# Optimization experiments

Measured on AMD Instinct MI355X. Metric: run time of the kernel, lower is better.

## Reference

```python
import jax, jax.numpy as jnp
import numpy as np

B, L, R = 4, 2048, 1024        # batch, seq_len, residual_dim
HID, EXP, K = 64, 2, 3          # hidden_dim, expansion_factor, conv_kernel_size
D = HID * EXP                   # ssm_input_dim = 128
N = HID                         # SSM state size = 64


def setup_inputs() -> dict:
    key = jax.random.key(0)
    ks = jax.random.split(key, 16)
    g = lambda k, s: jax.random.normal(k, s, dtype=jnp.float32) * 0.02
    inp = {
        "up_x":   jax.random.normal(ks[0], (B, L, R), dtype=jnp.float32),
        "W_up":   g(ks[1], (R, 2 * D)),
        "b_up":   g(ks[2], (2 * D,)),
        "conv_w": g(ks[3], (D, K)),          # depthwise Conv1d weight [C,1,K] squeezed
        "conv_b": g(ks[4], (D,)),
        "W_delta": g(ks[5], (D, D)),
        "b_delta": g(ks[6], (D,)),
        "W_B":    g(ks[7], (D, N)),
        "b_B":    g(ks[8], (N,)),
        "W_C":    g(ks[9], (D, N)),
        "b_C":    g(ks[10], (N,)),
        "A_log":  jnp.log(jnp.broadcast_to(jnp.arange(1, N + 1, dtype=jnp.float32), (D, N))),
        "D_skip": jnp.ones((D,), dtype=jnp.float32),
        "W_down": g(ks[11], (D, R)),
        "b_down": g(ks[12], (R,)),
    }
    return inp


def reference(up_x, W_up, b_up, conv_w, conv_b, W_delta, b_delta,
              W_B, b_B, W_C, b_C, A_log, D_skip, W_down, b_down):
    Lq = up_x.shape[1]
    u = up_x @ W_up + b_up                               # [B,L,2D]
    left, right = jnp.split(u, 2, axis=-1)               # each [B,L,D]

    # causal depthwise conv (pad left K-1, truncate to L)
    xp = jnp.pad(left, ((0, 0), (K - 1, 0), (0, 0)))     # [B,L+K-1,D]
    conv = sum(conv_w[:, k] * xp[:, k:k + Lq, :] for k in range(K)) + conv_b
    x = jax.nn.silu(conv)                                # [B,L,D]

    # S6 selective scan
    delta = jax.nn.softplus(x @ W_delta + b_delta)       # [B,L,D]
    Bm = x @ W_B + b_B                                   # [B,L,N]
    Cm = x @ W_C + b_C                                   # [B,L,N]
    A = -jnp.exp(A_log)                                  # [D,N]
    dA = jnp.exp(delta[..., None] * A)                   # [B,L,D,N]
    dBx = delta[..., None] * Bm[:, :, None, :] * x[..., None]  # [B,L,D,N]

    def step(h, inputs):
        dA_t, dBx_t, C_t = inputs                        # [B,D,N],[B,D,N],[B,N]
        h = dA_t * h + dBx_t
        y_t = jnp.einsum('bdn,bn->bd', h, C_t)
        return h, y_t

    h0 = jnp.zeros((up_x.shape[0], D, N), dtype=x.dtype)
    _, ys = jax.lax.scan(step, h0, (jnp.swapaxes(dA, 0, 1),
                                    jnp.swapaxes(dBx, 0, 1),
                                    jnp.swapaxes(Cm, 0, 1)))
    y = jnp.swapaxes(ys, 0, 1) + D_skip * x              # [B,L,D]

    gated = y * jax.nn.silu(right)                       # SiLU gate
    return gated @ W_down + b_down                       # [B,L,R]
```

## Files before the change

### kernel.cpp

```cpp
#include <hip/hip_runtime.h>
#include <math.h>

#define B_ 4
#define L_ 2048
#define R_ 1024
#define D_ 128
#define N_ 64
#define TWO_D 256
#define M_ (B_*L_)

#define LSTR 68

typedef __attribute__((ext_vector_type(8))) short bf16x8;
typedef __attribute__((ext_vector_type(4))) float f32x4;

__device__ __forceinline__ float silu_f(float z) {
    return z / (1.0f + __expf(-z));
}

__device__ __forceinline__ float softplus_f(float z) {
    return fmaxf(z, 0.0f) + log1pf(__expf(-fabsf(z)));
}

__device__ __forceinline__ short f2bf(float f) {
    union { float f; unsigned int u; } v; v.f = f;
    unsigned int r = v.u + 0x7FFF + ((v.u >> 16) & 1);
    return (short)(r >> 16);
}

__device__ __forceinline__ bf16x8 pack8(float4 a, float4 b) {
    bf16x8 r;
    r[0] = f2bf(a.x); r[1] = f2bf(a.y); r[2] = f2bf(a.z); r[3] = f2bf(a.w);
    r[4] = f2bf(b.x); r[5] = f2bf(b.y); r[6] = f2bf(b.z); r[7] = f2bf(b.w);
    return r;
}

__global__ __launch_bounds__(256) void gemm_up_splitk(
    const float* __restrict__ A,
    const float* __restrict__ W,
    float* __restrict__ P0,
    float* __restrict__ P1)
{
    __shared__ short Al[64 * LSTR];
    __shared__ short Bl[64 * LSTR];

    int lid = blockIdx.x;
    int xcd = lid & 7;
    int slot = lid >> 3;
    int bm = xcd * 16 + (slot >> 3);
    int r3 = slot & 7;
    int bn = r3 & 3;
    int split = r3 >> 2;
    float* P = split ? P1 : P0;
    int k0 = split * 512;

    int tid = threadIdx.x;
    int w = tid >> 6, l = tid & 63;
    int lm = l & 15, q = l >> 4;
    int wm = (w & 1) * 32, wn = (w >> 1) * 32;

    f32x4 acc00 = {0,0,0,0}, acc01 = {0,0,0,0}, acc10 = {0,0,0,0}, acc11 = {0,0,0,0};

    int ar = tid >> 2, ak = (tid & 3) * 8;
    int bcol = tid & 63, bk = (tid >> 6) * 8;

    const float* Ag = A + (size_t)(bm * 64 + ar) * 1024 + k0 + ak;
    const float* Wg = W + (size_t)(k0) * TWO_D + (size_t)bn * 64 + bcol;

    for (int kt = 0; kt < 512; kt += 32) {
        float4 a0 = *(const float4*)(Ag + kt);
        float4 a1 = *(const float4*)(Ag + kt + 4);
        *(bf16x8*)&Al[ar * LSTR + ak] = pack8(a0, a1);

        float w0 = Wg[(size_t)(kt + bk + 0) * TWO_D];
        float w1 = Wg[(size_t)(kt + bk + 1) * TWO_D];
        float w2 = Wg[(size_t)(kt + bk + 2) * TWO_D];
        float w3 = Wg[(size_t)(kt + bk + 3) * TWO_D];
        float w4 = Wg[(size_t)(kt + bk + 4) * TWO_D];
        float w5 = Wg[(size_t)(kt + bk + 5) * TWO_D];
        float w6 = Wg[(size_t)(kt + bk + 6) * TWO_D];
        float w7 = Wg[(size_t)(kt + bk + 7) * TWO_D];
        *(bf16x8*)&Bl[bcol * LSTR + bk] =
            pack8(make_float4(w0, w1, w2, w3), make_float4(w4, w5, w6, w7));

        __syncthreads();

        bf16x8 af0 = *(bf16x8*)&Al[(wm + lm) * LSTR + q * 8];
        bf16x8 af1 = *(bf16x8*)&Al[(wm + 16 + lm) * LSTR + q * 8];
        bf16x8 bf0 = *(bf16x8*)&Bl[(wn + lm) * LSTR + q * 8];
        bf16x8 bf1 = *(bf16x8*)&Bl[(wn + 16 + lm) * LSTR + q * 8];

        acc00 = __builtin_amdgcn_mfma_f32_16x16x32_bf16(af0, bf0, acc00, 0, 0, 0);
        acc01 = __builtin_amdgcn_mfma_f32_16x16x32_bf16(af0, bf1, acc01, 0, 0, 0);
        acc10 = __builtin_amdgcn_mfma_f32_16x16x32_bf16(af1, bf0, acc10, 0, 0, 0);
        acc11 = __builtin_amdgcn_mfma_f32_16x16x32_bf16(af1, bf1, acc11, 0, 0, 0);

        __syncthreads();
    }

    #pragma unroll
    for (int i = 0; i < 4; i++) {
        int r0 = bm * 64 + wm + q * 4 + i;
        int r1 = r0 + 16;
        int c0 = bn * 64 + wn + lm;
        int c1 = c0 + 16;
        P[(size_t)r0 * TWO_D + c0] = acc00[i];
        P[(size_t)r0 * TWO_D + c1] = acc01[i];
        P[(size_t)r1 * TWO_D + c0] = acc10[i];
        P[(size_t)r1 * TWO_D + c1] = acc11[i];
    }
}

__global__ __launch_bounds__(256) void conv_gate_kernel(
    const float* __restrict__ P0,
    const float* __restrict__ P1,
    const float* __restrict__ b_up,
    const float* __restrict__ conv_w,
    const float* __restrict__ conv_b,
    float* __restrict__ x,
    float* __restrict__ u)
{
    int idx = blockIdx.x * 256 + threadIdx.x;
    int r = idx >> 8;
    int c = idx & 255;
    float bb = b_up[c];
    float p = P0[idx] + P1[idx] + bb;

    if (c >= 128) {
        u[idx] = p;
        return;
    }
    int t = r & (L_ - 1);
    float w0 = conv_w[c * 3 + 0];
    float w1 = conv_w[c * 3 + 1];
    float w2 = conv_w[c * 3 + 2];
    float v1 = (t >= 1) ? P0[idx - 256] + P1[idx - 256] + bb : 0.0f;
    float v0 = (t >= 2) ? P0[idx - 512] + P1[idx - 512] + bb : 0.0f;
    float z = fmaf(w0, v0, fmaf(w1, v1, fmaf(w2, p, conv_b[c])));
    x[(size_t)r * D_ + c] = silu_f(z);
}

__global__ __launch_bounds__(256) void proj_mfma(
    const float* __restrict__ x,
    const float* __restrict__ W_delta, const float* __restrict__ b_delta,
    const float* __restrict__ W_B,     const float* __restrict__ b_B,
    const float* __restrict__ W_C,     const float* __restrict__ b_C,
    float* __restrict__ delta,
    float* __restrict__ Bm,
    float* __restrict__ Cm)
{
    __shared__ short Al[64 * LSTR];
    __shared__ short Bl[64 * LSTR];

    int lid = blockIdx.x;
    int xcd = lid & 7;
    int slot = lid >> 3;
    int bm = xcd * 16 + (slot >> 2);
    int bn = slot & 3;

    const float* Wsel; const float* bsel; int wstride;
    if (bn < 2)       { Wsel = W_delta + bn * 64; bsel = b_delta + bn * 64; wstride = 128; }
    else if (bn == 2) { Wsel = W_B;               bsel = b_B;               wstride = 64;  }
    else              { Wsel = W_C;               bsel = b_C;               wstride = 64;  }

    int tid = threadIdx.x;
    int w = tid >> 6, l = tid & 63;
    int lm = l & 15, q = l >> 4;
    int wm = (w & 1) * 32, wn = (w >> 1) * 32;

    f32x4 acc00 = {0,0,0,0}, acc01 = {0,0,0,0}, acc10 = {0,0,0,0}, acc11 = {0,0,0,0};

    int ar = tid >> 2, ak = (tid & 3) * 8;
    int bcol = tid & 63, bk = (tid >> 6) * 8;

    const float* Ag = x + (size_t)(bm * 64 + ar) * D_ + ak;
    const float* Wg = Wsel + bcol;

    for (int kt = 0; kt < 128; kt += 32) {
        float4 a0 = *(const float4*)(Ag + kt);
        float4 a1 = *(const float4*)(Ag + kt + 4);
        *(bf16x8*)&Al[ar * LSTR + ak] = pack8(a0, a1);

        float w0 = Wg[(size_t)(kt + bk + 0) * wstride];
        float w1 = Wg[(size_t)(kt + bk + 1) * wstride];
        float w2 = Wg[(size_t)(kt + bk + 2) * wstride];
        float w3 = Wg[(size_t)(kt + bk + 3) * wstride];
        float w4 = Wg[(size_t)(kt + bk + 4) * wstride];
        float w5 = Wg[(size_t)(kt + bk + 5) * wstride];
        float w6 = Wg[(size_t)(kt + bk + 6) * wstride];
        float w7 = Wg[(size_t)(kt + bk + 7) * wstride];
        *(bf16x8*)&Bl[bcol * LSTR + bk] =
            pack8(make_float4(w0, w1, w2, w3), make_float4(w4, w5, w6, w7));

        __syncthreads();

        bf16x8 af0 = *(bf16x8*)&Al[(wm + lm) * LSTR + q * 8];
        bf16x8 af1 = *(bf16x8*)&Al[(wm + 16 + lm) * LSTR + q * 8];
        bf16x8 bf0 = *(bf16x8*)&Bl[(wn + lm) * LSTR + q * 8];
        bf16x8 bf1 = *(bf16x8*)&Bl[(wn + 16 + lm) * LSTR + q * 8];

        acc00 = __builtin_amdgcn_mfma_f32_16x16x32_bf16(af0, bf0, acc00, 0, 0, 0);
        acc01 = __builtin_amdgcn_mfma_f32_16x16x32_bf16(af0, bf1, acc01, 0, 0, 0);
        acc10 = __builtin_amdgcn_mfma_f32_16x16x32_bf16(af1, bf0, acc10, 0, 0, 0);
        acc11 = __builtin_amdgcn_mfma_f32_16x16x32_bf16(af1, bf1, acc11, 0, 0, 0);

        __syncthreads();
    }

    #pragma unroll
    for (int i = 0; i < 4; i++) {
        int r0 = bm * 64 + wm + q * 4 + i;
        int r1 = r0 + 16;
        int c0 = wn + lm;
        int c1 = c0 + 16;
        float v00 = acc00[i] + bsel[c0];
        float v01 = acc01[i] + bsel[c1];
        float v10 = acc10[i] + bsel[c0];
        float v11 = acc11[i] + bsel[c1];
        if (bn < 2) {
            int cc0 = bn * 64 + c0, cc1 = bn * 64 + c1;
            delta[(size_t)r0 * D_ + cc0] = softplus_f(v00);
            delta[(size_t)r0 * D_ + cc1] = softplus_f(v01);
            delta[(size_t)r1 * D_ + cc0] = softplus_f(v10);
            delta[(size_t)r1 * D_ + cc1] = softplus_f(v11);
        } else if (bn == 2) {
            Bm[(size_t)r0 * N_ + c0] = v00;
            Bm[(size_t)r0 * N_ + c1] = v01;
            Bm[(size_t)r1 * N_ + c0] = v10;
            Bm[(size_t)r1 * N_ + c1] = v11;
        } else {
            Cm[(size_t)r0 * N_ + c0] = v00;
            Cm[(size_t)r0 * N_ + c1] = v01;
            Cm[(size_t)r1 * N_ + c0] = v10;
            Cm[(size_t)r1 * N_ + c1] = v11;
        }
    }
}

template<int LOG_NC>
__global__ __launch_bounds__(256) void scan_sumA(
    const float* __restrict__ delta,
    const float* __restrict__ x,
    const float* __restrict__ Bm,
    const float* __restrict__ A_log,
    float* __restrict__ ch_aprod,
    float* __restrict__ ch_h)
{
    constexpr int NCt = 1 << LOG_NC;
    constexpr int TCt = L_ >> LOG_NC;

    int wid = blockIdx.x * 4 + (threadIdx.x >> 6);
    int l = threadIdx.x & 63;
    int g = l >> 4, j = l & 15;
    int c = wid & (NCt - 1);
    int dq = (wid >> LOG_NC) & 31;
    int b = wid >> (LOG_NC + 5);
    int d = dq * 4 + g;

    const float LOG2E = 1.44269504089f;
    float4 Ar = *(const float4*)&A_log[d * N_ + j * 4];
    float Ai0 = -__expf(Ar.x) * LOG2E;
    float Ai1 = -__expf(Ar.y) * LOG2E;
    float Ai2 = -__expf(Ar.z) * LOG2E;
    float Ai3 = -__expf(Ar.w) * LOG2E;

    size_t row0 = (size_t)b * L_ + c * TCt;
    const float* dp = delta + row0 * D_ + d;
    const float* xp = x     + row0 * D_ + d;
    const float* bp = Bm    + row0 * N_ + j * 4;

    float h0 = 0, h1 = 0, h2 = 0, h3 = 0;
    float S = 0;

    #pragma unroll 8
    for (int t = 0; t < TCt; t++) {
        float dl = dp[t * D_];
        float xv = xp[t * D_];
        float4 bv = *(const float4*)&bp[t * N_];
        float e0 = exp2f(dl * Ai0);
        float e1 = exp2f(dl * Ai1);
        float e2 = exp2f(dl * Ai2);
        float e3 = exp2f(dl * Ai3);
        float dbx = dl * xv;
        h0 = fmaf(e0, h0, dbx * bv.x);
        h1 = fmaf(e1, h1, dbx * bv.y);
        h2 = fmaf(e2, h2, dbx * bv.z);
        h3 = fmaf(e3, h3, dbx * bv.w);
        S += dl;
    }

    size_t ci = (((size_t)b * D_ + d) * NCt + c) * N_ + j * 4;
    *(float4*)&ch_aprod[ci] = make_float4(exp2f(Ai0 * S), exp2f(Ai1 * S),
                                          exp2f(Ai2 * S), exp2f(Ai3 * S));
    *(float4*)&ch_h[ci]     = make_float4(h0, h1, h2, h3);
}

template<int LOG_NC>
__global__ __launch_bounds__(256) void scan_prefix(
    float* __restrict__ aprod_hin,
    const float* __restrict__ ch_h)
{
    constexpr int NCt = 1 << LOG_NC;
    int idx = blockIdx.x * 256 + threadIdx.x;
    int n = idx & 63;
    int rest = idx >> 6;
    size_t base = (size_t)rest * NCt * N_ + n;
    float h = 0.0f;
    #pragma unroll 8
    for (int c = 0; c < NCt; c++) {
        size_t o = base + (size_t)c * N_;
        float a  = aprod_hin[o];
        float hh = ch_h[o];
        aprod_hin[o] = h;
        h = fmaf(a, h, hh);
    }
}

template<int LOG_NC>
__global__ __launch_bounds__(256) void scan_outB(
    const float* __restrict__ delta,
    const float* __restrict__ x,
    const float* __restrict__ Bm,
    const float* __restrict__ Cm,
    const float* __restrict__ A_log,
    const float* __restrict__ D_skip,
    const float* __restrict__ hin,
    float* __restrict__ y)
{
    constexpr int NCt = 1 << LOG_NC;
    constexpr int TCt = L_ >> LOG_NC;

    int wid = blockIdx.x * 4 + (threadIdx.x >> 6);
    int l = threadIdx.x & 63;
    int g = l >> 4, j = l & 15;
    int c = wid & (NCt - 1);
    int dq = (wid >> LOG_NC) & 31;
    int b = wid >> (LOG_NC + 5);
    int d = dq * 4 + g;

    const float LOG2E = 1.44269504089f;
    float4 Ar = *(const float4*)&A_log[d * N_ + j * 4];
    float Ai0 = -__expf(Ar.x) * LOG2E;
    float Ai1 = -__expf(Ar.y) * LOG2E;
    float Ai2 = -__expf(Ar.z) * LOG2E;
    float Ai3 = -__expf(Ar.w) * LOG2E;
    float dsk = D_skip[d];

    float4 hv = *(const float4*)&hin[(((size_t)b * D_ + d) * NCt + c) * N_ + j * 4];
    float h0 = hv.x, h1 = hv.y, h2 = hv.z, h3 = hv.w;

    size_t row0 = (size_t)b * L_ + c * TCt;
    const float* dp = delta + row0 * D_ + d;
    const float* xp = x     + row0 * D_ + d;
    const float* bp = Bm    + row0 * N_ + j * 4;
    const float* cp = Cm    + row0 * N_ + j * 4;
    float*       yp = y     + row0 * D_ + d;

    #pragma unroll 8
    for (int t = 0; t < TCt; t++) {
        float dl = dp[t * D_];
        float xv = xp[t * D_];
        float4 bv = *(const float4*)&bp[t * N_];
        float4 cv = *(const float4*)&cp[t * N_];
        float e0 = exp2f(dl * Ai0);
        float e1 = exp2f(dl * Ai1);
        float e2 = exp2f(dl * Ai2);
        float e3 = exp2f(dl * Ai3);
        float dbx = dl * xv;
        h0 = fmaf(e0, h0, dbx * bv.x);
        h1 = fmaf(e1, h1, dbx * bv.y);
        h2 = fmaf(e2, h2, dbx * bv.z);
        h3 = fmaf(e3, h3, dbx * bv.w);
        float p = fmaf(h0, cv.x, fmaf(h1, cv.y, fmaf(h2, cv.z, h3 * cv.w)));
        p += __shfl_xor(p, 1, 64);
        p += __shfl_xor(p, 2, 64);
        p += __shfl_xor(p, 4, 64);
        p += __shfl_xor(p, 8, 64);
        if (j == 0) yp[t * D_] = fmaf(dsk, xv, p);
    }
}

__global__ __launch_bounds__(256) void gemm_down_mfma(
    const float* __restrict__ y,
    const float* __restrict__ u,
    const float* __restrict__ W,
    const float* __restrict__ bias,
    float* __restrict__ out)
{
    __shared__ short Al[64 * LSTR];
    __shared__ short Bl[64 * LSTR];

    int lid = blockIdx.x;
    int xcd = lid & 7;
    int slot = lid >> 3;
    int bm = xcd * 16 + (slot >> 4);
    int bn = slot & 15;

    int tid = threadIdx.x;
    int w = tid >> 6, l = tid & 63;
    int lm = l & 15, q = l >> 4;
    int wm = (w & 1) * 32, wn = (w >> 1) * 32;

    f32x4 acc00 = {0,0,0,0}, acc01 = {0,0,0,0}, acc10 = {0,0,0,0}, acc11 = {0,0,0,0};

    int ar = tid >> 2, ak = (tid & 3) * 8;
    int bcol = tid & 63, bk = (tid >> 6) * 8;

    const float* Yg = y + (size_t)(bm * 64 + ar) * D_ + ak;
    const float* Ug = u + (size_t)(bm * 64 + ar) * TWO_D + D_ + ak;
    const float* Wg = W + (size_t)bn * 64 + bcol;

    for (int kt = 0; kt < 128; kt += 32) {
        float4 y0 = *(const float4*)(Yg + kt);
        float4 y1 = *(const float4*)(Yg + kt + 4);
        float4 g0 = *(const float4*)(Ug + kt);
        float4 g1 = *(const float4*)(Ug + kt + 4);
        float4 a0 = make_float4(y0.x * silu_f(g0.x), y0.y * silu_f(g0.y),
                                y0.z * silu_f(g0.z), y0.w * silu_f(g0.w));
        float4 a1 = make_float4(y1.x * silu_f(g1.x), y1.y * silu_f(g1.y),
                                y1.z * silu_f(g1.z), y1.w * silu_f(g1.w));
        *(bf16x8*)&Al[ar * LSTR + ak] = pack8(a0, a1);

        float w0 = Wg[(size_t)(kt + bk + 0) * R_];
        float w1 = Wg[(size_t)(kt + bk + 1) * R_];
        float w2 = Wg[(size_t)(kt + bk + 2) * R_];
        float w3 = Wg[(size_t)(kt + bk + 3) * R_];
        float w4 = Wg[(size_t)(kt + bk + 4) * R_];
        float w5 = Wg[(size_t)(kt + bk + 5) * R_];
        float w6 = Wg[(size_t)(kt + bk + 6) * R_];
        float w7 = Wg[(size_t)(kt + bk + 7) * R_];
        *(bf16x8*)&Bl[bcol * LSTR + bk] =
            pack8(make_float4(w0, w1, w2, w3), make_float4(w4, w5, w6, w7));

        __syncthreads();

        bf16x8 af0 = *(bf16x8*)&Al[(wm + lm) * LSTR + q * 8];
        bf16x8 af1 = *(bf16x8*)&Al[(wm + 16 + lm) * LSTR + q * 8];
        bf16x8 bf0 = *(bf16x8*)&Bl[(wn + lm) * LSTR + q * 8];
        bf16x8 bf1 = *(bf16x8*)&Bl[(wn + 16 + lm) * LSTR + q * 8];

        acc00 = __builtin_amdgcn_mfma_f32_16x16x32_bf16(af0, bf0, acc00, 0, 0, 0);
        acc01 = __builtin_amdgcn_mfma_f32_16x16x32_bf16(af0, bf1, acc01, 0, 0, 0);
        acc10 = __builtin_amdgcn_mfma_f32_16x16x32_bf16(af1, bf0, acc10, 0, 0, 0);
        acc11 = __builtin_amdgcn_mfma_f32_16x16x32_bf16(af1, bf1, acc11, 0, 0, 0);

        __syncthreads();
    }

    #pragma unroll
    for (int i = 0; i < 4; i++) {
        int r0 = bm * 64 + wm + q * 4 + i;
        int r1 = r0 + 16;
        int c0 = bn * 64 + wn + lm;
        int c1 = c0 + 16;
        out[(size_t)r0 * R_ + c0] = acc00[i] + bias[c0];
        out[(size_t)r0 * R_ + c1] = acc01[i] + bias[c1];
        out[(size_t)r1 * R_ + c0] = acc10[i] + bias[c0];
        out[(size_t)r1 * R_ + c1] = acc11[i] + bias[c1];
    }
}

extern "C" void kernel_launch(void* const* d_in, const int* in_sizes, int n_in,
                              void* d_out, int out_size, void* d_ws, size_t ws_size,
                              hipStream_t stream)
{
    const float* up_x    = (const float*)d_in[0];
    const float* W_up    = (const float*)d_in[1];
    const float* b_up    = (const float*)d_in[2];
    const float* conv_w  = (const float*)d_in[3];
    const float* conv_b  = (const float*)d_in[4];
    const float* W_delta = (const float*)d_in[5];
    const float* b_delta = (const float*)d_in[6];
    const float* W_B     = (const float*)d_in[7];
    const float* b_B     = (const float*)d_in[8];
    const float* W_C     = (const float*)d_in[9];
    const float* b_C     = (const float*)d_in[10];
    const float* A_log   = (const float*)d_in[11];
    const float* D_skip  = (const float*)d_in[12];
    const float* W_down  = (const float*)d_in[13];
    const float* b_down  = (const float*)d_in[14];

    float* out = (float*)d_out;
    float* ws  = (float*)d_ws;

    float* u     = ws;
    float* x     = u + (size_t)M_ * TWO_D;
    float* delta = x + (size_t)M_ * D_;
    float* Bm    = delta + (size_t)M_ * D_;
    float* Cm    = Bm + (size_t)M_ * N_;
    float* y     = Cm + (size_t)M_ * N_;
    float* ch_aprod = y + (size_t)M_ * D_;
    bool big = ws_size >= (size_t)41943040;

    float* P0 = delta;
    float* P1 = y;

    gemm_up_splitk<<<1024, 256, 0, stream>>>(up_x, W_up, P0, P1);

    conv_gate_kernel<<<(M_ * TWO_D) / 256, 256, 0, stream>>>(
        P0, P1, b_up, conv_w, conv_b, x, u);

    proj_mfma<<<4 * (M_ / 64), 256, 0, stream>>>(
        x, W_delta, b_delta, W_B, b_B, W_C, b_C, delta, Bm, Cm);

    if (big) {
        constexpr int LNC = 6;
        float* ch_h = ch_aprod + (size_t)B_ * D_ * (1 << LNC) * N_;
        scan_sumA<LNC><<<(B_ * (D_ / 4) * (1 << LNC)) / 4, 256, 0, stream>>>(
            delta, x, Bm, A_log, ch_aprod, ch_h);
        scan_prefix<LNC><<<(B_ * D_ * N_) / 256, 256, 0, stream>>>(
            ch_aprod, ch_h);
        scan_outB<LNC><<<(B_ * (D_ / 4) * (1 << LNC)) / 4, 256, 0, stream>>>(
            delta, x, Bm, Cm, A_log, D_skip, ch_aprod, y);
    } else {
        constexpr int LNC = 5;
        float* ch_h = ch_aprod + (size_t)B_ * D_ * (1 << LNC) * N_;
        scan_sumA<LNC><<<(B_ * (D_ / 4) * (1 << LNC)) / 4, 256, 0, stream>>>(
            delta, x, Bm, A_log, ch_aprod, ch_h);
        scan_prefix<LNC><<<(B_ * D_ * N_) / 256, 256, 0, stream>>>(
            ch_aprod, ch_h);
        scan_outB<LNC><<<(B_ * (D_ / 4) * (1 << LNC)) / 4, 256, 0, stream>>>(
            delta, x, Bm, Cm, A_log, D_skip, ch_aprod, y);
    }

    gemm_down_mfma<<<16 * (M_ / 64), 256, 0, stream>>>(
        y, u, W_down, b_down, out);
}
```

Baseline: 218.7 us.

## Fuse causal conv+SiLU into projection GEMM and fix scan chunk count

Merges the conv/gate elementwise kernel into the delta/B/C projection GEMM. Each block reduces the split-K partials for its 64 rows plus a 2-row halo into shared memory, applies the depthwise conv and SiLU, and feeds the bf16 result straight to MFMA. This removes one launch and the round-trip of x through global memory before the GEMM. The cost is that all four column blocks redundantly recompute the conv, and that the split-K partial buffers move to separate workspace. The scan now always uses 64 chunks, dropping the workspace-size fallback to 32, which assumes the workspace is large enough.

```diff
diff --git a/kernel.cpp b/kernel.cpp
--- a/kernel.cpp
+++ b/kernel.cpp
@@ -9,7 +9,11 @@
 #define TWO_D 256
 #define M_ (B_*L_)
 
+#define LNC 6
+#define NC 64
+
 #define LSTR 68
+#define LSTRX 136
 
 typedef __attribute__((ext_vector_type(8))) short bf16x8;
 typedef __attribute__((ext_vector_type(4))) float f32x4;
@@ -65,7 +69,7 @@
     int bcol = tid & 63, bk = (tid >> 6) * 8;
 
     const float* Ag = A + (size_t)(bm * 64 + ar) * 1024 + k0 + ak;
-    const float* Wg = W + (size_t)(k0) * TWO_D + (size_t)bn * 64 + bcol;
+    const float* Wg = W + (size_t)k0 * TWO_D + (size_t)bn * 64 + bcol;
 
     for (int kt = 0; kt < 512; kt += 32) {
         float4 a0 = *(const float4*)(Ag + kt);
@@ -111,45 +115,23 @@
     }
 }
 
-__global__ __launch_bounds__(256) void conv_gate_kernel(
+__global__ __launch_bounds__(256) void convproj_mfma(
     const float* __restrict__ P0,
     const float* __restrict__ P1,
     const float* __restrict__ b_up,
     const float* __restrict__ conv_w,
     const float* __restrict__ conv_b,
-    float* __restrict__ x,
-    float* __restrict__ u)
-{
-    int idx = blockIdx.x * 256 + threadIdx.x;
-    int r = idx >> 8;
-    int c = idx & 255;
-    float bb = b_up[c];
-    float p = P0[idx] + P1[idx] + bb;
-
-    if (c >= 128) {
-        u[idx] = p;
-        return;
-    }
-    int t = r & (L_ - 1);
-    float w0 = conv_w[c * 3 + 0];
-    float w1 = conv_w[c * 3 + 1];
-    float w2 = conv_w[c * 3 + 2];
-    float v1 = (t >= 1) ? P0[idx - 256] + P1[idx - 256] + bb : 0.0f;
-    float v0 = (t >= 2) ? P0[idx - 512] + P1[idx - 512] + bb : 0.0f;
-    float z = fmaf(w0, v0, fmaf(w1, v1, fmaf(w2, p, conv_b[c])));
-    x[(size_t)r * D_ + c] = silu_f(z);
-}
-
-__global__ __launch_bounds__(256) void proj_mfma(
-    const float* __restrict__ x,
     const float* __restrict__ W_delta, const float* __restrict__ b_delta,
     const float* __restrict__ W_B,     const float* __restrict__ b_B,
     const float* __restrict__ W_C,     const float* __restrict__ b_C,
+    float* __restrict__ x,
+    float* __restrict__ u,
     float* __restrict__ delta,
     float* __restrict__ Bm,
     float* __restrict__ Cm)
 {
-    __shared__ short Al[64 * LSTR];
+    __shared__ float uu[66 * 128];
+    __shared__ short Xl[64 * LSTRX];
     __shared__ short Bl[64 * LSTR];
 
     int lid = blockIdx.x;
@@ -157,30 +139,100 @@
     int slot = lid >> 3;
     int bm = xcd * 16 + (slot >> 2);
     int bn = slot & 3;
+    int tid = threadIdx.x;
+
+    bool seq_start = (bm & 31) == 0;
+
+    #pragma unroll
+    for (int i = 0; i < 9; i++) {
+        int fi = tid + i * 256;
+        if (fi < 2112) {
+            int row = fi >> 5;
+            int c4 = (fi & 31) * 4;
+            int gr = bm * 64 + row - 2;
+            float4 v;
+            if (seq_start && row < 2) {
+                v = make_float4(0.f, 0.f, 0.f, 0.f);
+            } else {
+                size_t gi = (size_t)gr * TWO_D + c4;
+                float4 p0 = *(const float4*)&P0[gi];
+                float4 p1 = *(const float4*)&P1[gi];
+                float4 bb = *(const float4*)&b_up[c4];
+                v = make_float4(p0.x + p1.x + bb.x, p0.y + p1.y + bb.y,
+                                p0.z + p1.z + bb.z, p0.w + p1.w + bb.w);
+            }
+            *(float4*)&uu[fi * 4] = v;
+        }
+    }
+
+    if (bn == 1) {
+        #pragma unroll
+        for (int i = 0; i < 8; i++) {
+            int fi = tid + i * 256;
+            int row = fi >> 5;
+            int c4 = (fi & 31) * 4 + 128;
+            int gr = bm * 64 + row;
+            size_t gi = (size_t)gr * TWO_D + c4;
+            float4 p0 = *(const float4*)&P0[gi];
+            float4 p1 = *(const float4*)&P1[gi];
+            float4 bb = *(const float4*)&b_up[c4];
+            *(float4*)&u[gi] = make_float4(p0.x + p1.x + bb.x, p0.y + p1.y + bb.y,
+                                           p0.z + p1.z + bb.z, p0.w + p1.w + bb.w);
+        }
+    }
+    __syncthreads();
+
+    #pragma unroll
+    for (int i = 0; i < 8; i++) {
+        int fi = tid + i * 256;
+        int row = fi >> 5;
+        int c4 = (fi & 31) * 4;
+        float4 v2 = *(const float4*)&uu[(row + 2) * 128 + c4];
+        float4 v1 = *(const float4*)&uu[(row + 1) * 128 + c4];
+        float4 v0 = *(const float4*)&uu[(row + 0) * 128 + c4];
+        float4 z;
+        {
+            float w0 = conv_w[(c4 + 0) * 3 + 0], w1 = conv_w[(c4 + 0) * 3 + 1], w2 = conv_w[(c4 + 0) * 3 + 2];
+            z.x = silu_f(fmaf(w0, v0.x, fmaf(w1, v1.x, fmaf(w2, v2.x, conv_b[c4 + 0]))));
+        }
+        {
+            float w0 = conv_w[(c4 + 1) * 3 + 0], w1 = conv_w[(c4 + 1) * 3 + 1], w2 = conv_w[(c4 + 1) * 3 + 2];
+            z.y = silu_f(fmaf(w0, v0.y, fmaf(w1, v1.y, fmaf(w2, v2.y, conv_b[c4 + 1]))));
+        }
+        {
+            float w0 = conv_w[(c4 + 2) * 3 + 0], w1 = conv_w[(c4 + 2) * 3 + 1], w2 = conv_w[(c4 + 2) * 3 + 2];
+            z.z = silu_f(fmaf(w0, v0.z, fmaf(w1, v1.z, fmaf(w2, v2.z, conv_b[c4 + 2]))));
+        }
+        {
+            float w0 = conv_w[(c4 + 3) * 3 + 0], w1 = conv_w[(c4 + 3) * 3 + 1], w2 = conv_w[(c4 + 3) * 3 + 2];
+            z.w = silu_f(fmaf(w0, v0.w, fmaf(w1, v1.w, fmaf(w2, v2.w, conv_b[c4 + 3]))));
+        }
+        short4 zb;
+        zb.x = f2bf(z.x); zb.y = f2bf(z.y); zb.z = f2bf(z.z); zb.w = f2bf(z.w);
+        *(short4*)&Xl[row * LSTRX + c4] = zb;
+        if (bn == 0) {
+            int gr = bm * 64 + row;
+            *(float4*)&x[(size_t)gr * D_ + c4] = z;
+        }
+    }
 
     const float* Wsel; const float* bsel; int wstride;
     if (bn < 2)       { Wsel = W_delta + bn * 64; bsel = b_delta + bn * 64; wstride = 128; }
     else if (bn == 2) { Wsel = W_B;               bsel = b_B;               wstride = 64;  }
     else              { Wsel = W_C;               bsel = b_C;               wstride = 64;  }
 
-    int tid = threadIdx.x;
     int w = tid >> 6, l = tid & 63;
     int lm = l & 15, q = l >> 4;
     int wm = (w & 1) * 32, wn = (w >> 1) * 32;
 
     f32x4 acc00 = {0,0,0,0}, acc01 = {0,0,0,0}, acc10 = {0,0,0,0}, acc11 = {0,0,0,0};
 
-    int ar = tid >> 2, ak = (tid & 3) * 8;
     int bcol = tid & 63, bk = (tid >> 6) * 8;
-
-    const float* Ag = x + (size_t)(bm * 64 + ar) * D_ + ak;
     const float* Wg = Wsel + bcol;
 
+    __syncthreads();
+
     for (int kt = 0; kt < 128; kt += 32) {
-        float4 a0 = *(const float4*)(Ag + kt);
-        float4 a1 = *(const float4*)(Ag + kt + 4);
-        *(bf16x8*)&Al[ar * LSTR + ak] = pack8(a0, a1);
-
         float w0 = Wg[(size_t)(kt + bk + 0) * wstride];
         float w1 = Wg[(size_t)(kt + bk + 1) * wstride];
         float w2 = Wg[(size_t)(kt + bk + 2) * wstride];
@@ -194,8 +246,8 @@
 
         __syncthreads();
 
-        bf16x8 af0 = *(bf16x8*)&Al[(wm + lm) * LSTR + q * 8];
-        bf16x8 af1 = *(bf16x8*)&Al[(wm + 16 + lm) * LSTR + q * 8];
+        bf16x8 af0 = *(bf16x8*)&Xl[(wm + lm) * LSTRX + kt + q * 8];
+        bf16x8 af1 = *(bf16x8*)&Xl[(wm + 16 + lm) * LSTRX + kt + q * 8];
         bf16x8 bf0 = *(bf16x8*)&Bl[(wn + lm) * LSTR + q * 8];
         bf16x8 bf1 = *(bf16x8*)&Bl[(wn + 16 + lm) * LSTR + q * 8];
 
@@ -237,7 +289,6 @@
     }
 }
 
-template<int LOG_NC>
 __global__ __launch_bounds__(256) void scan_sumA(
     const float* __restrict__ delta,
     const float* __restrict__ x,
@@ -246,15 +297,14 @@
     float* __restrict__ ch_aprod,
     float* __restrict__ ch_h)
 {
-    constexpr int NCt = 1 << LOG_NC;
-    constexpr int TCt = L_ >> LOG_NC;
+    constexpr int TCt = L_ >> LNC;
 
     int wid = blockIdx.x * 4 + (threadIdx.x >> 6);
     int l = threadIdx.x & 63;
     int g = l >> 4, j = l & 15;
-    int c = wid & (NCt - 1);
-    int dq = (wid >> LOG_NC) & 31;
-    int b = wid >> (LOG_NC + 5);
+    int c = wid & (NC - 1);
+    int dq = (wid >> LNC) & 31;
+    int b = wid >> (LNC + 5);
     int d = dq * 4 + g;
 
     const float LOG2E = 1.44269504089f;
@@ -289,25 +339,23 @@
         S += dl;
     }
 
-    size_t ci = (((size_t)b * D_ + d) * NCt + c) * N_ + j * 4;
+    size_t ci = (((size_t)b * D_ + d) * NC + c) * N_ + j * 4;
     *(float4*)&ch_aprod[ci] = make_float4(exp2f(Ai0 * S), exp2f(Ai1 * S),
                                           exp2f(Ai2 * S), exp2f(Ai3 * S));
     *(float4*)&ch_h[ci]     = make_float4(h0, h1, h2, h3);
 }
 
-template<int LOG_NC>
 __global__ __launch_bounds__(256) void scan_prefix(
     float* __restrict__ aprod_hin,
     const float* __restrict__ ch_h)
 {
-    constexpr int NCt = 1 << LOG_NC;
     int idx = blockIdx.x * 256 + threadIdx.x;
     int n = idx & 63;
     int rest = idx >> 6;
-    size_t base = (size_t)rest * NCt * N_ + n;
+    size_t base = (size_t)rest * NC * N_ + n;
     float h = 0.0f;
     #pragma unroll 8
-    for (int c = 0; c < NCt; c++) {
+    for (int c = 0; c < NC; c++) {
         size_t o = base + (size_t)c * N_;
         float a  = aprod_hin[o];
         float hh = ch_h[o];
@@ -316,7 +364,6 @@
     }
 }
 
-template<int LOG_NC>
 __global__ __launch_bounds__(256) void scan_outB(
     const float* __restrict__ delta,
     const float* __restrict__ x,
@@ -327,15 +374,14 @@
     const float* __restrict__ hin,
     float* __restrict__ y)
 {
-    constexpr int NCt = 1 << LOG_NC;
-    constexpr int TCt = L_ >> LOG_NC;
+    constexpr int TCt = L_ >> LNC;
 
     int wid = blockIdx.x * 4 + (threadIdx.x >> 6);
     int l = threadIdx.x & 63;
     int g = l >> 4, j = l & 15;
-    int c = wid & (NCt - 1);
-    int dq = (wid >> LOG_NC) & 31;
-    int b = wid >> (LOG_NC + 5);
+    int c = wid & (NC - 1);
+    int dq = (wid >> LNC) & 31;
+    int b = wid >> (LNC + 5);
     int d = dq * 4 + g;
 
     const float LOG2E = 1.44269504089f;
@@ -346,7 +392,7 @@
     float Ai3 = -__expf(Ar.w) * LOG2E;
     float dsk = D_skip[d];
 
-    float4 hv = *(const float4*)&hin[(((size_t)b * D_ + d) * NCt + c) * N_ + j * 4];
+    float4 hv = *(const float4*)&hin[(((size_t)b * D_ + d) * NC + c) * N_ + j * 4];
     float h0 = hv.x, h1 = hv.y, h2 = hv.z, h3 = hv.w;
 
     size_t row0 = (size_t)b * L_ + c * TCt;
@@ -490,38 +536,23 @@
     float* Cm    = Bm + (size_t)M_ * N_;
     float* y     = Cm + (size_t)M_ * N_;
     float* ch_aprod = y + (size_t)M_ * D_;
-    bool big = ws_size >= (size_t)41943040;
-
-    float* P0 = delta;
-    float* P1 = y;
+    float* ch_h  = ch_aprod + (size_t)B_ * D_ * NC * N_;
+    float* P0    = ch_h + (size_t)B_ * D_ * NC * N_;
+    float* P1    = P0 + (size_t)M_ * TWO_D;
 
     gemm_up_splitk<<<1024, 256, 0, stream>>>(up_x, W_up, P0, P1);
 
-    conv_gate_kernel<<<(M_ * TWO_D) / 256, 256, 0, stream>>>(
-        P0, P1, b_up, conv_w, conv_b, x, u);
-
-    proj_mfma<<<4 * (M_ / 64), 256, 0, stream>>>(
-        x, W_delta, b_delta, W_B, b_B, W_C, b_C, delta, Bm, Cm);
-
-    if (big) {
-        constexpr int LNC = 6;
-        float* ch_h = ch_aprod + (size_t)B_ * D_ * (1 << LNC) * N_;
-        scan_sumA<LNC><<<(B_ * (D_ / 4) * (1 << LNC)) / 4, 256, 0, stream>>>(
-            delta, x, Bm, A_log, ch_aprod, ch_h);
-        scan_prefix<LNC><<<(B_ * D_ * N_) / 256, 256, 0, stream>>>(
-            ch_aprod, ch_h);
-        scan_outB<LNC><<<(B_ * (D_ / 4) * (1 << LNC)) / 4, 256, 0, stream>>>(
-            delta, x, Bm, Cm, A_log, D_skip, ch_aprod, y);
-    } else {
-        constexpr int LNC = 5;
-        float* ch_h = ch_aprod + (size_t)B_ * D_ * (1 << LNC) * N_;
-        scan_sumA<LNC><<<(B_ * (D_ / 4) * (1 << LNC)) / 4, 256, 0, stream>>>(
-            delta, x, Bm, A_log, ch_aprod, ch_h);
-        scan_prefix<LNC><<<(B_ * D_ * N_) / 256, 256, 0, stream>>>(
-            ch_aprod, ch_h);
-        scan_outB<LNC><<<(B_ * (D_ / 4) * (1 << LNC)) / 4, 256, 0, stream>>>(
-            delta, x, Bm, Cm, A_log, D_skip, ch_aprod, y);
-    }
+    convproj_mfma<<<512, 256, 0, stream>>>(
+        P0, P1, b_up, conv_w, conv_b,
+        W_delta, b_delta, W_B, b_B, W_C, b_C,
+        x, u, delta, Bm, Cm);
+
+    scan_sumA<<<(B_ * (D_ / 4) * NC) / 4, 256, 0, stream>>>(
+        delta, x, Bm, A_log, ch_aprod, ch_h);
+    scan_prefix<<<(B_ * D_ * N_) / 256, 256, 0, stream>>>(
+        ch_aprod, ch_h);
+    scan_outB<<<(B_ * (D_ / 4) * NC) / 4, 256, 0, stream>>>(
+        delta, x, Bm, Cm, A_log, D_skip, ch_aprod, y);
 
     gemm_down_mfma<<<16 * (M_ / 64), 256, 0, stream>>>(
         y, u, W_down, b_down, out);
```

Result: no change. 218.6 us (-0.0%).
